# Kernel tuning notes

Hardware: AMD Instinct MI355X
Metric: run time of the kernel (lower is better)

The kernel has to match this reference:

```python
import jax, jax.numpy as jnp
import numpy as np

B, N, C, D = 4, 4096, 1024, 32  # batch, tokens, channels, head dim
EPS = 1e-15
PAD_VAL = 1.0


def setup_inputs() -> dict:
    key = jax.random.key(0)
    k1, k2, k3 = jax.random.split(key, 3)
    x = jax.random.normal(k1, (B, N, C), dtype=jnp.float32)
    W_qkv = jax.random.normal(k2, (3 * C, C), dtype=jnp.float32) * 0.02
    W_proj = jax.random.normal(k3, (C, C), dtype=jnp.float32) * 0.02
    b_proj = jnp.zeros((C,), dtype=jnp.float32)
    return {"x": x, "W_qkv": W_qkv, "W_proj": W_proj, "b_proj": b_proj}


def reference(x, W_qkv, W_proj, b_proj):
    Bx, Nx, Cx = x.shape
    h = Cx // D
    # qkv projection (no bias), then split as torch: reshape(B,N,3,C).permute(0,2,3,1)
    qkv = jnp.einsum('bnc,oc->bno', x, W_qkv)            # [B,N,3C]
    qkv = qkv.reshape(Bx, Nx, 3, Cx).transpose(0, 2, 3, 1)  # [B,3,C,N]
    q, k, v = qkv[:, 0], qkv[:, 1], qkv[:, 2]
    q = jax.nn.relu(q.reshape(Bx, h, D, Nx))             # [B,h,D,N]
    k = jax.nn.relu(k.reshape(Bx, h, D, Nx)).transpose(0, 1, 3, 2)  # [B,h,N,D]
    v = v.reshape(Bx, h, D, Nx)                          # [B,h,D,N]
    # pad v with a row of PAD_VAL=1 to carry the normalizer
    v = jnp.concatenate([v, jnp.full((Bx, h, 1, Nx), PAD_VAL, v.dtype)], axis=2)  # [B,h,D+1,N]
    vk = jnp.einsum('bhdn,bhne->bhde', v, k)             # [B,h,D+1,D]
    out = jnp.einsum('bhde,bhen->bhdn', vk, q)           # [B,h,D+1,N]
    out = out[:, :, :-1] / (out[:, :, -1:] + EPS)        # [B,h,D,N]
    out = out.reshape(Bx, Cx, Nx).transpose(0, 2, 1)     # [B,N,C]
    return jnp.einsum('bnc,oc->bno', out, W_proj) + b_proj
```

## Files before the change

kernel.cpp:

```cpp
#include <hip/hip_runtime.h>


using us8   = __attribute__((ext_vector_type(8))) unsigned short;
using us4   = __attribute__((ext_vector_type(4))) unsigned short;
using s8v   = __attribute__((ext_vector_type(8))) short;
using f32x4 = __attribute__((ext_vector_type(4))) float;

__device__ __forceinline__ unsigned short f2bf(float f) {
    union { float f; unsigned int u; } c; c.f = f;
    unsigned int r = c.u + 0x7fffu + ((c.u >> 16) & 1u);
    return (unsigned short)(r >> 16);
}
__device__ __forceinline__ float bf2f(unsigned short u) {
    union { unsigned int u; float f; } c; c.u = ((unsigned int)u) << 16;
    return c.f;
}

__device__ __forceinline__ void async16(const unsigned short* g, unsigned short* l) {
    __builtin_amdgcn_global_load_lds(
        (const __attribute__((address_space(1))) unsigned int*)g,
        (__attribute__((address_space(3))) unsigned int*)l, 16, 0, 0);
}

__global__ __launch_bounds__(256)
void prep(const float* __restrict__ x, const float* __restrict__ wq,
          const float* __restrict__ wp, unsigned short* __restrict__ xb,
          unsigned short* __restrict__ wqb, unsigned short* __restrict__ wpb,
          float* __restrict__ vkws) {
    const int NX = 16777216 / 8, NQ = 3145728 / 8, NP = 1048576 / 8, NZ = 135168 / 8;
    int gid = blockIdx.x * 256 + threadIdx.x;
    const float* in; unsigned short* out; int i;
    if (gid < NX)                    { in = x;  out = xb;  i = gid * 8; }
    else if (gid < NX + NQ)          { in = wq; out = wqb; i = (gid - NX) * 8; }
    else if (gid < NX + NQ + NP)     { in = wp; out = wpb; i = (gid - NX - NQ) * 8; }
    else if (gid < NX + NQ + NP + NZ) {
        int z = (gid - NX - NQ - NP) * 8;
        f32x4 zero = {};
        *(f32x4*)(vkws + z) = zero; *(f32x4*)(vkws + z + 4) = zero;
        return;
    } else return;
    float4 a = *(const float4*)(in + i);
    float4 b = *(const float4*)(in + i + 4);
    us8 o;
    o[0] = f2bf(a.x); o[1] = f2bf(a.y); o[2] = f2bf(a.z); o[3] = f2bf(a.w);
    o[4] = f2bf(b.x); o[5] = f2bf(b.y); o[6] = f2bf(b.z); o[7] = f2bf(b.w);
    *(us8*)(out + i) = o;
}

constexpr int HSZ = 128 * 64;

#define FENCE() asm volatile("" ::: "memory")
#define BARX()  do { FENCE(); __builtin_amdgcn_s_barrier(); FENCE(); } while (0)
#define LGKM0() asm volatile("s_waitcnt lgkmcnt(0)" ::: "memory")

#define MFMA_QUAD(MB, NB)                                                    \
  do {                                                                       \
    __builtin_amdgcn_s_setprio(1);                                           \
    _Pragma("unroll")                                                        \
    for (int mi_ = 0; mi_ < 4; ++mi_)                                        \
      _Pragma("unroll")                                                      \
      for (int ni_ = 0; ni_ < 2; ++ni_)                                      \
        _Pragma("unroll")                                                    \
        for (int kk_ = 0; kk_ < 2; ++kk_)                                    \
          acc[(MB) + mi_][(NB) + ni_] =                                      \
              __builtin_amdgcn_mfma_f32_16x16x32_bf16(                       \
                  af[mi_][kk_], bf[(NB) + ni_][kk_],                         \
                  acc[(MB) + mi_][(NB) + ni_], 0, 0, 0);                     \
    __builtin_amdgcn_s_setprio(0);                                           \
  } while (0)

__device__ __forceinline__
void stage_half(const unsigned short* __restrict__ G, int rowBase, int kcol,
                unsigned short* ldsHalf, int row0, int esw, int wv) {
    async16(G + (size_t)(rowBase + row0) * 1024 + kcol + esw,
            ldsHalf + wv * 512);
    async16(G + (size_t)(rowBase + 64 + row0) * 1024 + kcol + esw,
            ldsHalf + 4096 + wv * 512);
}

template <int MODE>
__device__ __forceinline__
void gemm_core256(const unsigned short* __restrict__ A,
                  const unsigned short* __restrict__ Bt,
                  unsigned short* __restrict__ Cq,
                  unsigned short* __restrict__ kvT,
                  float* __restrict__ Cf, const float* __restrict__ bias,
                  int N, int tM, int tN, unsigned short* lds) {
    unsigned short* As = lds;
    unsigned short* Bs = lds + 4 * HSZ;

    const int t    = threadIdx.x;
    const int lane = t & 63;
    const int wv   = t >> 6;
    const int wr   = wv >> 2;
    const int wc   = wv & 3;
    const int mrow = lane & 15;
    const int kq   = lane >> 4;
    const int m7   = lane & 7;

    const int row0 = t >> 3;
    const int esw  = ((t & 7) ^ (row0 & 7)) * 8;

    const int ks0 = ((0 * 4 + kq) ^ m7) * 8;
    const int ks1 = ((1 * 4 + kq) ^ m7) * 8;
    const int browB = wc * 32;

    f32x4 acc[8][4] = {};
    s8v af[4][2], bf[4][2];

    constexpr int NT = 16;

    stage_half(A,  tM,       0,  As + 0 * HSZ, row0, esw, wv);
    stage_half(A,  tM + 128, 0,  As + 1 * HSZ, row0, esw, wv);
    stage_half(Bt, tN,       0,  Bs + 0 * HSZ, row0, esw, wv);
    stage_half(Bt, tN + 128, 0,  Bs + 1 * HSZ, row0, esw, wv);
    stage_half(Bt, tN,       64, Bs + 2 * HSZ, row0, esw, wv);
    stage_half(Bt, tN + 128, 64, Bs + 3 * HSZ, row0, esw, wv);
    stage_half(A,  tM,       64, As + 2 * HSZ, row0, esw, wv);
    asm volatile("s_waitcnt vmcnt(6)" ::: "memory");
    BARX();

    for (int g = 0; g < NT; ++g) {
        const int c = g & 1;
        const unsigned short* Ard  = As + (c * 2 + wr) * HSZ;
        const unsigned short* B0rd = Bs + (c * 2 + 0) * HSZ;
        const unsigned short* B1rd = Bs + (c * 2 + 1) * HSZ;
        const int kt1 = (g + 1 < NT ? g + 1 : NT - 1) * 64;
        const int kt2 = (g + 2 < NT ? g + 2 : NT - 1) * 64;

        bf[0][0] = *(const s8v*)&B0rd[(browB + mrow) * 64 + ks0];
        bf[0][1] = *(const s8v*)&B0rd[(browB + mrow) * 64 + ks1];
        bf[1][0] = *(const s8v*)&B0rd[(browB + 16 + mrow) * 64 + ks0];
        bf[1][1] = *(const s8v*)&B0rd[(browB + 16 + mrow) * 64 + ks1];
#pragma unroll
        for (int mi = 0; mi < 4; ++mi) {
            af[mi][0] = *(const s8v*)&Ard[(mi * 16 + mrow) * 64 + ks0];
            af[mi][1] = *(const s8v*)&Ard[(mi * 16 + mrow) * 64 + ks1];
        }
        stage_half(A, tM + 128, kt1, As + ((c ^ 1) * 2 + 1) * HSZ, row0, esw, wv);
        BARX();
        LGKM0();
        MFMA_QUAD(0, 0);
        BARX();

        bf[2][0] = *(const s8v*)&B1rd[(browB + mrow) * 64 + ks0];
        bf[2][1] = *(const s8v*)&B1rd[(browB + mrow) * 64 + ks1];
        bf[3][0] = *(const s8v*)&B1rd[(browB + 16 + mrow) * 64 + ks0];
        bf[3][1] = *(const s8v*)&B1rd[(browB + 16 + mrow) * 64 + ks1];
        stage_half(Bt, tN, kt2, Bs + (c * 2 + 0) * HSZ, row0, esw, wv);
        BARX();
        LGKM0();
        MFMA_QUAD(0, 2);
        BARX();

#pragma unroll
        for (int mi = 0; mi < 4; ++mi) {
            af[mi][0] = *(const s8v*)&Ard[(64 + mi * 16 + mrow) * 64 + ks0];
            af[mi][1] = *(const s8v*)&Ard[(64 + mi * 16 + mrow) * 64 + ks1];
        }
        stage_half(Bt, tN + 128, kt2, Bs + (c * 2 + 1) * HSZ, row0, esw, wv);
        BARX();
        LGKM0();
        MFMA_QUAD(4, 0);
        BARX();

        stage_half(A, tM, kt2, As + (c * 2 + 0) * HSZ, row0, esw, wv);
        BARX();
        MFMA_QUAD(4, 2);
        asm volatile("s_waitcnt vmcnt(6)" ::: "memory");
        BARX();
    }

    const int crow0 = kq * 4;
    const int ccol  = mrow;
    if (MODE == 0) {
        if (tN >= 1024) {
            const int b2  = tM >> 12;
            const int nb0 = (tM & 4095) + wr * 128;
#pragma unroll
            for (int mi = 0; mi < 8; ++mi) {
                const int nbase = nb0 + mi * 16 + crow0;
#pragma unroll
                for (int ni = 0; ni < 4; ++ni) {
                    const int col = tN + (ni >> 1) * 128 + wc * 32 + (ni & 1) * 16 + ccol;
                    f32x4 v = acc[mi][ni];
                    if (col < 2048) {
                        v[0] = fmaxf(v[0], 0.f); v[1] = fmaxf(v[1], 0.f);
                        v[2] = fmaxf(v[2], 0.f); v[3] = fmaxf(v[3], 0.f);
                    }
                    us4 o;
                    o[0] = f2bf(v[0]); o[1] = f2bf(v[1]);
                    o[2] = f2bf(v[2]); o[3] = f2bf(v[3]);
                    *(us4*)&kvT[((size_t)b2 * 2048 + (col - 1024)) * 4096 + nbase] = o;
                }
            }
        } else {
#pragma unroll
            for (int mi = 0; mi < 8; ++mi)
#pragma unroll
                for (int ni = 0; ni < 4; ++ni) {
                    const int row = tM + wr * 128 + mi * 16 + crow0;
                    const int col = tN + (ni >> 1) * 128 + wc * 32 + (ni & 1) * 16 + ccol;
#pragma unroll
                    for (int r2 = 0; r2 < 4; ++r2)
                        Cq[(size_t)(row + r2) * 1024 + col] =
                            f2bf(fmaxf(acc[mi][ni][r2], 0.f));
                }
        }
    } else {
#pragma unroll
        for (int mi = 0; mi < 8; ++mi)
#pragma unroll
            for (int ni = 0; ni < 4; ++ni) {
                const int row = tM + wr * 128 + mi * 16 + crow0;
                const int col = tN + (ni >> 1) * 128 + wc * 32 + (ni & 1) * 16 + ccol;
#pragma unroll
                for (int r2 = 0; r2 < 4; ++r2)
                    Cf[(size_t)(row + r2) * N + col] = acc[mi][ni][r2] + bias[col];
            }
    }
    asm volatile("s_waitcnt vmcnt(0)" ::: "memory");
}

__device__ __forceinline__ void xcd_map256(int blk, int MT, int& tM, int& tN) {
    const int xcd = blk & 7;
    const int i   = blk >> 3;
    const int MTx = MT >> 3;
    const int ppan = MTx * 4;
    const int p   = i / ppan;
    const int i2  = i % ppan;
    tM = (xcd * MTx + (i2 >> 2)) * 256;
    tN = (p * 4 + (i2 & 3)) * 256;
}

__global__ __launch_bounds__(512, 2)
void gemm_qkv(const unsigned short* __restrict__ A,
              const unsigned short* __restrict__ Bt,
              unsigned short* __restrict__ Cq, unsigned short* __restrict__ kvT,
              int M, int N) {
    extern __shared__ unsigned short lds[];
    int tM, tN;
    xcd_map256(blockIdx.x, M >> 8, tM, tN);
    gemm_core256<0>(A, Bt, Cq, kvT, nullptr, nullptr, N, tM, tN, lds);
}

__global__ __launch_bounds__(512, 2)
void gemm_proj(const unsigned short* __restrict__ A,
               const unsigned short* __restrict__ Bt,
               float* __restrict__ C, const float* __restrict__ bias,
               int M, int N) {
    extern __shared__ unsigned short lds[];
    int tM, tN;
    xcd_map256(blockIdx.x, M >> 8, tM, tN);
    gemm_core256<1>(A, Bt, nullptr, nullptr, C, bias, N, tM, tN, lds);
}

__global__ __launch_bounds__(256)
void lite_vk(const unsigned short* __restrict__ kvT, float* __restrict__ vkws) {
    const int bh = blockIdx.x, ck = blockIdx.y;
    const int b = bh >> 5, h = bh & 31;
    const int S = 136;
    __shared__ unsigned short Ks[32 * S];
    __shared__ unsigned short Vs[32 * S];
    __shared__ float Rs[4][1088];
    const int t = threadIdx.x, lane = t & 63, wv = t >> 6;
    const unsigned short* Kp = kvT + ((size_t)b * 2048 + h * 32) * 4096 + ck * 512;
    const unsigned short* Vp = kvT + ((size_t)b * 2048 + 1024 + h * 32) * 4096 + ck * 512;
    const int sr = t >> 3, ss = (t & 7) * 16;
    f32x4 acc00 = {}, acc01 = {}, acc10 = {}, acc11 = {}, accO0 = {}, accO1 = {};
    s8v ones;
#pragma unroll
    for (int j = 0; j < 8; ++j) ones[j] = (short)0x3F80;
    const int mrow = lane & 15, kq = (lane >> 4) * 8;

    for (int tile = 0; tile < 4; ++tile) {
        int go = tile * 128 + ss;
        us8 k0v = *(const us8*)(Kp + (size_t)sr * 4096 + go);
        us8 k1v = *(const us8*)(Kp + (size_t)sr * 4096 + go + 8);
        us8 v0v = *(const us8*)(Vp + (size_t)sr * 4096 + go);
        us8 v1v = *(const us8*)(Vp + (size_t)sr * 4096 + go + 8);
        __syncthreads();
        *(us8*)&Ks[sr * S + ss]     = k0v;
        *(us8*)&Ks[sr * S + ss + 8] = k1v;
        *(us8*)&Vs[sr * S + ss]     = v0v;
        *(us8*)&Vs[sr * S + ss + 8] = v1v;
        __syncthreads();
        int ko = wv * 32 + kq;
        s8v a0 = *(const s8v*)&Vs[(mrow)      * S + ko];
        s8v a1 = *(const s8v*)&Vs[(16 + mrow) * S + ko];
        s8v b0 = *(const s8v*)&Ks[(mrow)      * S + ko];
        s8v b1 = *(const s8v*)&Ks[(16 + mrow) * S + ko];
        acc00 = __builtin_amdgcn_mfma_f32_16x16x32_bf16(a0, b0, acc00, 0, 0, 0);
        acc01 = __builtin_amdgcn_mfma_f32_16x16x32_bf16(a0, b1, acc01, 0, 0, 0);
        acc10 = __builtin_amdgcn_mfma_f32_16x16x32_bf16(a1, b0, acc10, 0, 0, 0);
        acc11 = __builtin_amdgcn_mfma_f32_16x16x32_bf16(a1, b1, acc11, 0, 0, 0);
        accO0 = __builtin_amdgcn_mfma_f32_16x16x32_bf16(ones, b0, accO0, 0, 0, 0);
        accO1 = __builtin_amdgcn_mfma_f32_16x16x32_bf16(ones, b1, accO1, 0, 0, 0);
    }

    const int ccol = lane & 15, crow = (lane >> 4) * 4;
    float* R = Rs[wv];
#pragma unroll
    for (int r2 = 0; r2 < 4; ++r2) {
        R[(crow + r2) * 32 + ccol]           = acc00[r2];
        R[(crow + r2) * 32 + 16 + ccol]      = acc01[r2];
        R[(16 + crow + r2) * 32 + ccol]      = acc10[r2];
        R[(16 + crow + r2) * 32 + 16 + ccol] = acc11[r2];
    }
    if ((lane >> 4) == 0) {
        R[1024 + ccol]      = accO0[0];
        R[1024 + 16 + ccol] = accO1[0];
    }
    __syncthreads();
    float* vkb = vkws + bh * (33 * 32);
    for (int i = t; i < 1056; i += 256) {
        float s = Rs[0][i] + Rs[1][i] + Rs[2][i] + Rs[3][i];
        atomicAdd(&vkb[i], s);
    }
}

__global__ __launch_bounds__(256)
void lite_apply(const unsigned short* __restrict__ qb,
                const float* __restrict__ vkws,
                unsigned short* __restrict__ yb) {
    const int bh = blockIdx.x, nb = blockIdx.y;
    const int b = bh >> 5, h = bh & 31;
    __shared__ unsigned short vkh[48 * 32];
    __shared__ unsigned short vkl[48 * 32];
    const int t = threadIdx.x;
    for (int i = t; i < 48 * 32; i += 256) {
        float v = (i < 33 * 32) ? vkws[bh * (33 * 32) + i] : 0.f;
        unsigned short hi = f2bf(v);
        vkh[i] = hi;
        vkl[i] = f2bf(v - bf2f(hi));
    }
    __syncthreads();

    const int lane = t & 63, wv = t >> 6;
    const int col = lane & 15, quad = lane >> 4;
    s8v b0h = *(const s8v*)&vkh[(col)      * 32 + quad * 8];
    s8v b0l = *(const s8v*)&vkl[(col)      * 32 + quad * 8];
    s8v b1h = *(const s8v*)&vkh[(16 + col) * 32 + quad * 8];
    s8v b1l = *(const s8v*)&vkl[(16 + col) * 32 + quad * 8];
    s8v b2h = *(const s8v*)&vkh[(32 + col) * 32 + quad * 8];
    s8v b2l = *(const s8v*)&vkl[(32 + col) * 32 + quad * 8];

    const int ntile = nb * 256 + wv * 64;
#pragma unroll
    for (int mi = 0; mi < 4; ++mi) {
        int tok = ntile + mi * 16 + col;
        const unsigned short* qp =
            qb + (size_t)(b * 4096 + tok) * 1024 + h * 32 + quad * 8;
        s8v a = *(const s8v*)qp;
        f32x4 n0 = {}, n1 = {}, dd = {};
        n0 = __builtin_amdgcn_mfma_f32_16x16x32_bf16(b0h, a, n0, 0, 0, 0);
        n0 = __builtin_amdgcn_mfma_f32_16x16x32_bf16(b0l, a, n0, 0, 0, 0);
        n1 = __builtin_amdgcn_mfma_f32_16x16x32_bf16(b1h, a, n1, 0, 0, 0);
        n1 = __builtin_amdgcn_mfma_f32_16x16x32_bf16(b1l, a, n1, 0, 0, 0);
        dd = __builtin_amdgcn_mfma_f32_16x16x32_bf16(b2h, a, dd, 0, 0, 0);
        dd = __builtin_amdgcn_mfma_f32_16x16x32_bf16(b2l, a, dd, 0, 0, 0);
        float den  = __shfl(dd[0], col, 64);
        float rinv = 1.f / (den + 1e-15f);
        us4 o0, o1;
#pragma unroll
        for (int r = 0; r < 4; ++r) {
            o0[r] = f2bf(n0[r] * rinv);
            o1[r] = f2bf(n1[r] * rinv);
        }
        size_t o = (size_t)(b * 4096 + tok) * 1024 + h * 32;
        *(us4*)&yb[o + quad * 4]      = o0;
        *(us4*)&yb[o + 16 + quad * 4] = o1;
    }
}

extern "C" void kernel_launch(void* const* d_in, const int* in_sizes, int n_in,
                              void* d_out, int out_size, void* d_ws, size_t ws_size,
                              hipStream_t stream) {
    const float* x     = (const float*)d_in[0];
    const float* Wqkv  = (const float*)d_in[1];
    const float* Wproj = (const float*)d_in[2];
    const float* bproj = (const float*)d_in[3];
    float* out = (float*)d_out;

    const int M = 16384, Cdim = 1024, O1 = 3072;

    unsigned short* xb     = (unsigned short*)d_ws;
    unsigned short* wqkvb  = xb + (size_t)M * Cdim;
    unsigned short* wprojb = wqkvb + (size_t)O1 * Cdim;
    unsigned short* qb     = wprojb + (size_t)Cdim * Cdim;
    unsigned short* kvT    = qb + (size_t)M * Cdim;
    unsigned short* ybuf   = kvT + (size_t)4 * 2048 * 4096;
    float* vkws            = (float*)(ybuf + (size_t)M * Cdim);

    static int attr_done = 0;
    if (!attr_done) {
        hipFuncSetAttribute((const void*)gemm_qkv,
                            hipFuncAttributeMaxDynamicSharedMemorySize, 131072);
        hipFuncSetAttribute((const void*)gemm_proj,
                            hipFuncAttributeMaxDynamicSharedMemorySize, 131072);
        attr_done = 1;
    }

    const int PREP_GROUPS = (16777216 + 3145728 + 1048576 + 135168) / 8;
    prep<<<(PREP_GROUPS + 255) / 256, 256, 0, stream>>>(
        x, Wqkv, Wproj, xb, wqkvb, wprojb, vkws);

    gemm_qkv<<<(M / 256) * (O1 / 256), 512, 131072, stream>>>(
        xb, wqkvb, qb, kvT, M, O1);

    lite_vk<<<dim3(128, 8), 256, 0, stream>>>(kvT, vkws);
    lite_apply<<<dim3(128, 16), 256, 0, stream>>>(qb, vkws, ybuf);

    gemm_proj<<<(M / 256) * (Cdim / 256), 512, 131072, stream>>>(
        ybuf, wprojb, out, bproj, M, Cdim);
}
```

Baseline: 309.8 us.

## Restructure GEMM main loop to prefetch next-tile fragments and cut barriers

```diff
diff --git a/kernel.cpp b/kernel.cpp
--- a/kernel.cpp
+++ b/kernel.cpp
@@ -51,9 +51,8 @@
 
 #define FENCE() asm volatile("" ::: "memory")
 #define BARX()  do { FENCE(); __builtin_amdgcn_s_barrier(); FENCE(); } while (0)
-#define LGKM0() asm volatile("s_waitcnt lgkmcnt(0)" ::: "memory")
-
-#define MFMA_QUAD(MB, NB)                                                    \
+
+#define MFMA_QUAD2(AF, BF, MB, NB)                                           \
   do {                                                                       \
     __builtin_amdgcn_s_setprio(1);                                           \
     _Pragma("unroll")                                                        \
@@ -64,18 +63,16 @@
         for (int kk_ = 0; kk_ < 2; ++kk_)                                    \
           acc[(MB) + mi_][(NB) + ni_] =                                      \
               __builtin_amdgcn_mfma_f32_16x16x32_bf16(                       \
-                  af[mi_][kk_], bf[(NB) + ni_][kk_],                         \
+                  AF[mi_][kk_], BF[ni_][kk_],                                \
                   acc[(MB) + mi_][(NB) + ni_], 0, 0, 0);                     \
     __builtin_amdgcn_s_setprio(0);                                           \
   } while (0)
 
 __device__ __forceinline__
-void stage_half(const unsigned short* __restrict__ G, int rowBase, int kcol,
-                unsigned short* ldsHalf, int row0, int esw, int wv) {
-    async16(G + (size_t)(rowBase + row0) * 1024 + kcol + esw,
-            ldsHalf + wv * 512);
-    async16(G + (size_t)(rowBase + 64 + row0) * 1024 + kcol + esw,
-            ldsHalf + 4096 + wv * 512);
+void stage2(const unsigned short* gl, int kc, int roff,
+            unsigned short* region, int wv) {
+    async16(gl + kc + roff,         region + wv * 512);
+    async16(gl + kc + roff + 65536, region + 4096 + wv * 512);
 }
 
 template <int MODE>
@@ -100,74 +97,84 @@
 
     const int row0 = t >> 3;
     const int esw  = ((t & 7) ^ (row0 & 7)) * 8;
+    const unsigned short* Aglane = A  + (size_t)(tM + row0) * 1024 + esw;
+    const unsigned short* Bglane = Bt + (size_t)(tN + row0) * 1024 + esw;
 
     const int ks0 = ((0 * 4 + kq) ^ m7) * 8;
     const int ks1 = ((1 * 4 + kq) ^ m7) * 8;
     const int browB = wc * 32;
 
     f32x4 acc[8][4] = {};
-    s8v af[4][2], bf[4][2];
+    s8v afP[4][2], afQ[4][2], bf01[2][2], bf23[2][2];
 
     constexpr int NT = 16;
 
-    stage_half(A,  tM,       0,  As + 0 * HSZ, row0, esw, wv);
-    stage_half(A,  tM + 128, 0,  As + 1 * HSZ, row0, esw, wv);
-    stage_half(Bt, tN,       0,  Bs + 0 * HSZ, row0, esw, wv);
-    stage_half(Bt, tN + 128, 0,  Bs + 1 * HSZ, row0, esw, wv);
-    stage_half(Bt, tN,       64, Bs + 2 * HSZ, row0, esw, wv);
-    stage_half(Bt, tN + 128, 64, Bs + 3 * HSZ, row0, esw, wv);
-    stage_half(A,  tM,       64, As + 2 * HSZ, row0, esw, wv);
-    asm volatile("s_waitcnt vmcnt(6)" ::: "memory");
+    stage2(Aglane, 0,  0,      As + 0 * HSZ, wv);
+    stage2(Aglane, 0,  131072, As + 1 * HSZ, wv);
+    stage2(Bglane, 0,  0,      Bs + 0 * HSZ, wv);
+    stage2(Bglane, 0,  131072, Bs + 1 * HSZ, wv);
+    stage2(Aglane, 64, 0,      As + 2 * HSZ, wv);
+    stage2(Aglane, 64, 131072, As + 3 * HSZ, wv);
+    stage2(Bglane, 64, 0,      Bs + 2 * HSZ, wv);
+    stage2(Bglane, 64, 131072, Bs + 3 * HSZ, wv);
+    asm volatile("s_waitcnt vmcnt(8)" ::: "memory");
     BARX();
 
+    {
+        const unsigned short* A0r = As + wr * HSZ;
+#pragma unroll
+        for (int mi = 0; mi < 4; ++mi) {
+            afP[mi][0] = *(const s8v*)&A0r[(mi * 16 + mrow) * 64 + ks0];
+            afP[mi][1] = *(const s8v*)&A0r[(mi * 16 + mrow) * 64 + ks1];
+        }
+        bf01[0][0] = *(const s8v*)&Bs[(browB + mrow) * 64 + ks0];
+        bf01[0][1] = *(const s8v*)&Bs[(browB + mrow) * 64 + ks1];
+        bf01[1][0] = *(const s8v*)&Bs[(browB + 16 + mrow) * 64 + ks0];
+        bf01[1][1] = *(const s8v*)&Bs[(browB + 16 + mrow) * 64 + ks1];
+    }
+
     for (int g = 0; g < NT; ++g) {
-        const int c = g & 1;
+        const int c  = g & 1;
+        const int cn = c ^ 1;
         const unsigned short* Ard  = As + (c * 2 + wr) * HSZ;
-        const unsigned short* B0rd = Bs + (c * 2 + 0) * HSZ;
         const unsigned short* B1rd = Bs + (c * 2 + 1) * HSZ;
-        const int kt1 = (g + 1 < NT ? g + 1 : NT - 1) * 64;
+        const unsigned short* An   = As + (cn * 2 + wr) * HSZ;
+        const unsigned short* B0n  = Bs + (cn * 2 + 0) * HSZ;
         const int kt2 = (g + 2 < NT ? g + 2 : NT - 1) * 64;
 
-        bf[0][0] = *(const s8v*)&B0rd[(browB + mrow) * 64 + ks0];
-        bf[0][1] = *(const s8v*)&B0rd[(browB + mrow) * 64 + ks1];
-        bf[1][0] = *(const s8v*)&B0rd[(browB + 16 + mrow) * 64 + ks0];
-        bf[1][1] = *(const s8v*)&B0rd[(browB + 16 + mrow) * 64 + ks1];
+        bf23[0][0] = *(const s8v*)&B1rd[(browB + mrow) * 64 + ks0];
+        bf23[0][1] = *(const s8v*)&B1rd[(browB + mrow) * 64 + ks1];
+        bf23[1][0] = *(const s8v*)&B1rd[(browB + 16 + mrow) * 64 + ks0];
+        bf23[1][1] = *(const s8v*)&B1rd[(browB + 16 + mrow) * 64 + ks1];
+        MFMA_QUAD2(afP, bf01, 0, 0);
+        BARX();
+
+        stage2(Bglane, kt2, 0, Bs + (c * 2 + 0) * HSZ, wv);
 #pragma unroll
         for (int mi = 0; mi < 4; ++mi) {
-            af[mi][0] = *(const s8v*)&Ard[(mi * 16 + mrow) * 64 + ks0];
-            af[mi][1] = *(const s8v*)&Ard[(mi * 16 + mrow) * 64 + ks1];
+            afQ[mi][0] = *(const s8v*)&Ard[(64 + mi * 16 + mrow) * 64 + ks0];
+            afQ[mi][1] = *(const s8v*)&Ard[(64 + mi * 16 + mrow) * 64 + ks1];
         }
-        stage_half(A, tM + 128, kt1, As + ((c ^ 1) * 2 + 1) * HSZ, row0, esw, wv);
+        MFMA_QUAD2(afP, bf23, 0, 2);
         BARX();
-        LGKM0();
-        MFMA_QUAD(0, 0);
+
+        stage2(Bglane, kt2, 131072, Bs + (c * 2 + 1) * HSZ, wv);
+        MFMA_QUAD2(afQ, bf01, 4, 0);
         BARX();
 
-        bf[2][0] = *(const s8v*)&B1rd[(browB + mrow) * 64 + ks0];
-        bf[2][1] = *(const s8v*)&B1rd[(browB + mrow) * 64 + ks1];
-        bf[3][0] = *(const s8v*)&B1rd[(browB + 16 + mrow) * 64 + ks0];
-        bf[3][1] = *(const s8v*)&B1rd[(browB + 16 + mrow) * 64 + ks1];
-        stage_half(Bt, tN, kt2, Bs + (c * 2 + 0) * HSZ, row0, esw, wv);
-        BARX();
-        LGKM0();
-        MFMA_QUAD(0, 2);
-        BARX();
-
+        asm volatile("s_waitcnt vmcnt(4)" ::: "memory");
 #pragma unroll
         for (int mi = 0; mi < 4; ++mi) {
-            af[mi][0] = *(const s8v*)&Ard[(64 + mi * 16 + mrow) * 64 + ks0];
-            af[mi][1] = *(const s8v*)&Ard[(64 + mi * 16 + mrow) * 64 + ks1];
+            afP[mi][0] = *(const s8v*)&An[(mi * 16 + mrow) * 64 + ks0];
+            afP[mi][1] = *(const s8v*)&An[(mi * 16 + mrow) * 64 + ks1];
         }
-        stage_half(Bt, tN + 128, kt2, Bs + (c * 2 + 1) * HSZ, row0, esw, wv);
-        BARX();
-        LGKM0();
-        MFMA_QUAD(4, 0);
-        BARX();
-
-        stage_half(A, tM, kt2, As + (c * 2 + 0) * HSZ, row0, esw, wv);
-        BARX();
-        MFMA_QUAD(4, 2);
-        asm volatile("s_waitcnt vmcnt(6)" ::: "memory");
+        bf01[0][0] = *(const s8v*)&B0n[(browB + mrow) * 64 + ks0];
+        bf01[0][1] = *(const s8v*)&B0n[(browB + mrow) * 64 + ks1];
+        bf01[1][0] = *(const s8v*)&B0n[(browB + 16 + mrow) * 64 + ks0];
+        bf01[1][1] = *(const s8v*)&B0n[(browB + 16 + mrow) * 64 + ks1];
+        stage2(Aglane, kt2, 0,      As + (c * 2 + 0) * HSZ, wv);
+        stage2(Aglane, kt2, 131072, As + (c * 2 + 1) * HSZ, wv);
+        MFMA_QUAD2(afQ, bf23, 4, 2);
         BARX();
     }
 
```

After: 300.1 us. 3.1% less time.
